# Performance work log

Measured on AMD Instinct MI355X. Metric: run time of the kernel, lower is better.

Reference implementation:

```python
import jax, jax.numpy as jnp
from jax import lax
import numpy as np
import math

INPUT_DIM = 64
HIDDEN_DIM = 512
SEQ_LEN = 256
BATCH = 512
PRED_LEN = 24
NUM_TARGETS = 1


def setup_inputs() -> dict:
    key = jax.random.key(0)
    ks = jax.random.split(key, 10)
    stdv = 1.0 / math.sqrt(HIDDEN_DIM)
    u = lambda k, shape: jax.random.uniform(k, shape, jnp.float32, -stdv, stdv)
    return {
        "x": jax.random.normal(ks[0], (BATCH, SEQ_LEN, INPUT_DIM), jnp.float32),
        "Wa": u(ks[1], (INPUT_DIM, INPUT_DIM)),
        "Ua": u(ks[2], (2 * HIDDEN_DIM, INPUT_DIM)),
        "ba": jnp.zeros((INPUT_DIM,), jnp.float32),
        "Va": u(ks[3], (INPUT_DIM, INPUT_DIM)),
        "W_ih": u(ks[4], (4 * HIDDEN_DIM, INPUT_DIM)),
        "W_hh": u(ks[5], (4 * HIDDEN_DIM, HIDDEN_DIM)),
        "b_ih": u(ks[6], (4 * HIDDEN_DIM,)),
        "b_hh": u(ks[7], (4 * HIDDEN_DIM,)),
        "fc_w": u(ks[8], (PRED_LEN * NUM_TARGETS, HIDDEN_DIM)),
        "fc_b": u(ks[9], (PRED_LEN * NUM_TARGETS,)),
    }


def reference(x, Wa, Ua, ba, Va, W_ih, W_hh, b_ih, b_hh, fc_w, fc_b):
    B, S, D = x.shape
    H = W_hh.shape[1]

    def step(carry, x_t):
        h, c = carry  # [B,H] each
        # attention gate over input features
        hc = jnp.concatenate([h, c], axis=1)  # [B,2H]
        a_t = jnp.tanh(x_t @ Wa + hc @ Ua + ba) @ Va  # [B,D]
        alpha_t = jax.nn.softmax(a_t, axis=1)
        x_att = alpha_t * x_t
        # torch.nn.LSTMCell: gates in order i, f, g, o
        gates = x_att @ W_ih.T + h @ W_hh.T + b_ih + b_hh  # [B,4H]
        i, f, g, o = jnp.split(gates, 4, axis=1)
        c_new = jax.nn.sigmoid(f) * c + jax.nn.sigmoid(i) * jnp.tanh(g)
        h_new = jax.nn.sigmoid(o) * jnp.tanh(c_new)
        return (h_new, c_new), None

    h0 = jnp.zeros((B, H), x.dtype)
    c0 = jnp.zeros((B, H), x.dtype)
    (h_T, _), _ = lax.scan(step, (h0, c0), jnp.swapaxes(x, 0, 1))  # scan over seq
    y = h_T @ fc_w.T + fc_b  # [B, pred_len*num_targets]
    return y.reshape(B, PRED_LEN, NUM_TARGETS)
```

## Files before the change

kernel.cpp:

```cpp
#include <hip/hip_runtime.h>
#include <math.h>

#define B 512
#define S 256
#define D 64
#define H 512
#define BH (B*H)

typedef __attribute__((ext_vector_type(8))) short short8;
typedef __attribute__((ext_vector_type(4))) float f32x4;
typedef __attribute__((ext_vector_type(4))) unsigned int uint4v;

__device__ inline unsigned short f2bf(float v) {
    unsigned int u = __float_as_uint(v);
    unsigned int r = (u + 0x7fffu + ((u >> 16) & 1u)) >> 16;
    return (unsigned short)r;
}
__device__ inline float bf2f(unsigned short b) {
    return __uint_as_float(((unsigned int)b) << 16);
}


__global__ __launch_bounds__(256) void init_zero(
    float* __restrict__ h32, float* __restrict__ c32)
{
    int i = blockIdx.x * blockDim.x + threadIdx.x;
    if (i < BH) { h32[i] = 0.f; c32[i] = 0.f; }
}

__global__ __launch_bounds__(256) void prep_weights(
    const float* __restrict__ Whh, const float* __restrict__ Wih,
    unsigned short* __restrict__ wswz)
{
    const int jt = blockIdx.x;
    const int kb = blockIdx.y;
    const int t = threadIdx.x;
    const int jj = t >> 3;
    const int kk8 = t & 7;
    const int jg = jt*32 + jj;
    const int u = jg >> 2, q = jg & 3;
    const int Wrow = q*H + u;

    const float* src = (kb < 8) ? (Whh + (size_t)Wrow*H + kb*64 + kk8*8)
                                : (Wih + (size_t)Wrow*D + kk8*8);
    float v[8];
    *(float4*)&v[0] = *(const float4*)(src);
    *(float4*)&v[4] = *(const float4*)(src + 4);

    unsigned short hi[8], lo[8];
    #pragma unroll
    for (int e = 0; e < 8; ++e) {
        hi[e] = f2bf(v[e]);
        lo[e] = f2bf(v[e] - bf2f(hi[e]));
    }
    const int ks = kk8 >> 2, cg2 = kk8 & 3;
    const size_t slab = (size_t)(jt*9 + kb) * 4096;
    *(short8*)(wswz + slab + (size_t)(0*2048 + ks*1024 + cg2*256 + jj*8)) = *(const short8*)hi;
    *(short8*)(wswz + slab + (size_t)(1*2048 + ks*1024 + cg2*256 + jj*8)) = *(const short8*)lo;
}

__global__ __launch_bounds__(256) void attn_kernel(
    const float* __restrict__ x, const float* __restrict__ Wa,
    const float* __restrict__ Ua, const float* __restrict__ ba,
    const float* __restrict__ Va,
    const float* __restrict__ h32, const float* __restrict__ c32,
    float* __restrict__ xatt, int t)
{
    const int d = threadIdx.x & 63;
    const int r = (threadIdx.x >> 6) & 1;
    const int p = threadIdx.x >> 7;
    const int b = blockIdx.x * 2 + r;

    const int rd = t & 1;
    const float* __restrict__ hrow = h32 + (size_t)rd*BH + (size_t)b*H;
    const float* __restrict__ crow = c32 + (size_t)b*H;
    const float* __restrict__ xrow = x + ((size_t)b*S + t)*D;

    __shared__ float part[2][2][64];
    __shared__ float ta[2][64];
    __shared__ float pv[2][2][64];

    float a = 0.f;
    if (p == 0) {
        a = ba[d];
        #pragma unroll 8
        for (int k = 0; k < D; ++k) a += xrow[k] * Wa[k*D + d];
        #pragma unroll 8
        for (int k = 0; k < H; ++k) a += hrow[k] * Ua[k*D + d];
    } else {
        #pragma unroll 8
        for (int k = 0; k < H; ++k) a += crow[k] * Ua[(size_t)(H + k)*D + d];
    }
    part[r][p][d] = a;
    __syncthreads();
    if (p == 0) ta[r][d] = tanhf(part[r][0][d] + part[r][1][d]);
    __syncthreads();
    float av = 0.f;
    {
        const int k0 = p * 32;
        #pragma unroll 8
        for (int k = k0; k < k0 + 32; ++k) av += ta[r][k] * Va[k*D + d];
    }
    pv[r][p][d] = av;
    __syncthreads();
    float v = pv[r][0][d] + pv[r][1][d];
    float m = v;
    #pragma unroll
    for (int o = 32; o > 0; o >>= 1) m = fmaxf(m, __shfl_xor(m, o));
    float e = expf(v - m);
    float ssum = e;
    #pragma unroll
    for (int o = 32; o > 0; o >>= 1) ssum += __shfl_xor(ssum, o);
    if (p == 0) {
        xatt[(size_t)b*D + d] = (e / ssum) * xrow[d];
    }
}

__global__ __launch_bounds__(256, 2) void gates_kernel(
    const unsigned short* __restrict__ wswz,
    const float* __restrict__ xatt,
    float* __restrict__ h32, float* __restrict__ c32,
    const float* __restrict__ bih, const float* __restrict__ bhh, int t)
{
    const int tid = threadIdx.x;
    const int lane = tid & 63;
    const int wid = tid >> 6;
    const int wr = wid >> 1, wc = wid & 1;
    const int jt = blockIdx.x;
    const int b0 = blockIdx.y * 64;
    const int l15 = lane & 15;
    const int cgi = lane >> 4;

    __shared__ __align__(16) unsigned short aHi[2][64][72];
    __shared__ __align__(16) unsigned short aLo[2][64][72];
    __shared__ float gout[64][37];

    const int rd = t & 1, wrs = rd ^ 1;
    const float* __restrict__ h32r = h32 + (size_t)rd*BH;

    const int srow = tid >> 2;
    const int q4 = tid & 3;

    auto stage = [&](const float* src, int buf) {
        float v[16];
        #pragma unroll
        for (int i = 0; i < 4; ++i)
            *(float4*)&v[i*4] = *(const float4*)(src + i*4);
        unsigned int hp[8], lp[8];
        #pragma unroll
        for (int w = 0; w < 8; ++w) {
            unsigned int ue = __float_as_uint(v[2*w]);
            unsigned int uo = __float_as_uint(v[2*w+1]);
            hp[w] = (ue >> 16) | (uo & 0xFFFF0000u);
            float le = v[2*w]   - __uint_as_float(ue & 0xFFFF0000u);
            float lq = v[2*w+1] - __uint_as_float(uo & 0xFFFF0000u);
            lp[w] = (__float_as_uint(le) >> 16) | (__float_as_uint(lq) & 0xFFFF0000u);
        }
        *(uint4v*)&aHi[buf][srow][q4*16]     = *(uint4v*)&hp[0];
        *(uint4v*)&aHi[buf][srow][q4*16 + 8] = *(uint4v*)&hp[4];
        *(uint4v*)&aLo[buf][srow][q4*16]     = *(uint4v*)&lp[0];
        *(uint4v*)&aLo[buf][srow][q4*16 + 8] = *(uint4v*)&lp[4];
    };

    stage(h32r + (size_t)(b0 + srow)*H + q4*16, 0);
    __syncthreads();

    f32x4 acc0 = {0,0,0,0}, acc1 = {0,0,0,0};
    const int lofs = cgi*256 + (wc*16 + l15)*8;

    for (int kb = 0; kb < 9; ++kb) {
        const int cur = kb & 1;
        const unsigned short* pB = wswz + (size_t)(jt*9 + kb)*4096;
        short8 bh0 = *(const short8*)(pB + 0*2048 + 0*1024 + lofs);
        short8 bh1 = *(const short8*)(pB + 0*2048 + 1*1024 + lofs);
        short8 bl0 = *(const short8*)(pB + 1*2048 + 0*1024 + lofs);
        short8 bl1 = *(const short8*)(pB + 1*2048 + 1*1024 + lofs);
        if (kb < 8) {
            const float* nsrc = (kb + 1 < 8)
                ? (h32r + (size_t)(b0 + srow)*H + (kb + 1)*64 + q4*16)
                : (xatt + (size_t)(b0 + srow)*D + q4*16);
            stage(nsrc, cur ^ 1);
        }
        const int ar = wr*32 + l15;
        short8 ah00 = *(const short8*)&aHi[cur][ar     ][cgi*8];
        short8 ah01 = *(const short8*)&aHi[cur][ar     ][32 + cgi*8];
        short8 ah10 = *(const short8*)&aHi[cur][ar + 16][cgi*8];
        short8 ah11 = *(const short8*)&aHi[cur][ar + 16][32 + cgi*8];
        short8 al00 = *(const short8*)&aLo[cur][ar     ][cgi*8];
        short8 al01 = *(const short8*)&aLo[cur][ar     ][32 + cgi*8];
        short8 al10 = *(const short8*)&aLo[cur][ar + 16][cgi*8];
        short8 al11 = *(const short8*)&aLo[cur][ar + 16][32 + cgi*8];

        acc0 = __builtin_amdgcn_mfma_f32_16x16x32_bf16(ah00, bh0, acc0, 0,0,0);
        acc1 = __builtin_amdgcn_mfma_f32_16x16x32_bf16(ah10, bh0, acc1, 0,0,0);
        acc0 = __builtin_amdgcn_mfma_f32_16x16x32_bf16(ah00, bl0, acc0, 0,0,0);
        acc1 = __builtin_amdgcn_mfma_f32_16x16x32_bf16(ah10, bl0, acc1, 0,0,0);
        acc0 = __builtin_amdgcn_mfma_f32_16x16x32_bf16(al00, bh0, acc0, 0,0,0);
        acc1 = __builtin_amdgcn_mfma_f32_16x16x32_bf16(al10, bh0, acc1, 0,0,0);
        acc0 = __builtin_amdgcn_mfma_f32_16x16x32_bf16(ah01, bh1, acc0, 0,0,0);
        acc1 = __builtin_amdgcn_mfma_f32_16x16x32_bf16(ah11, bh1, acc1, 0,0,0);
        acc0 = __builtin_amdgcn_mfma_f32_16x16x32_bf16(ah01, bl1, acc0, 0,0,0);
        acc1 = __builtin_amdgcn_mfma_f32_16x16x32_bf16(ah11, bl1, acc1, 0,0,0);
        acc0 = __builtin_amdgcn_mfma_f32_16x16x32_bf16(al01, bh1, acc0, 0,0,0);
        acc1 = __builtin_amdgcn_mfma_f32_16x16x32_bf16(al11, bh1, acc1, 0,0,0);
        __syncthreads();
    }

    {
        const int m0 = cgi * 4;
        #pragma unroll
        for (int r = 0; r < 4; ++r) {
            gout[wr*32 + m0 + r     ][wc*16 + l15] = acc0[r];
            gout[wr*32 + 16 + m0 + r][wc*16 + l15] = acc1[r];
        }
    }
    __syncthreads();
    {
        const int u8 = tid & 7;
        const int u_glob = jt*8 + u8;
        const float bs0 = bih[0*H + u_glob] + bhh[0*H + u_glob];
        const float bs1 = bih[1*H + u_glob] + bhh[1*H + u_glob];
        const float bs2 = bih[2*H + u_glob] + bhh[2*H + u_glob];
        const float bs3 = bih[3*H + u_glob] + bhh[3*H + u_glob];
        float* __restrict__ h32w = h32 + (size_t)wrs*BH;
        #pragma unroll
        for (int pp = 0; pp < 2; ++pp) {
            const int row_loc = (tid >> 3) + pp*32;
            const int b = b0 + row_loc;
            float gi = gout[row_loc][u8*4 + 0] + bs0;
            float gf = gout[row_loc][u8*4 + 1] + bs1;
            float gg = gout[row_loc][u8*4 + 2] + bs2;
            float go = gout[row_loc][u8*4 + 3] + bs3;
            const size_t idx = (size_t)b*H + u_glob;
            float c_old = c32[idx];
            float si = 1.f/(1.f + expf(-gi));
            float sf = 1.f/(1.f + expf(-gf));
            float so = 1.f/(1.f + expf(-go));
            float cn = sf*c_old + si*tanhf(gg);
            float hn = so*tanhf(cn);
            c32[idx] = cn;
            h32w[idx] = hn;
        }
    }
}

__global__ __launch_bounds__(256) void fc_kernel(
    const float* __restrict__ fcw, const float* __restrict__ fcb,
    const float* __restrict__ h32, float* __restrict__ out)
{
    const int b = blockIdx.x;
    __shared__ float hrow[H];
    const float* __restrict__ hp = h32 + (size_t)b*H;
    for (int k = threadIdx.x; k < H; k += 256) hrow[k] = hp[k];
    __syncthreads();
    int j = threadIdx.x;
    if (j < 24) {
        float a = fcb[j];
        #pragma unroll 8
        for (int k = 0; k < H; ++k) a += hrow[k] * fcw[j*H + k];
        out[b*24 + j] = a;
    }
}

extern "C" void kernel_launch(void* const* d_in, const int* in_sizes, int n_in,
                              void* d_out, int out_size, void* d_ws, size_t ws_size,
                              hipStream_t stream) {
    const float* x   = (const float*)d_in[0];
    const float* Wa  = (const float*)d_in[1];
    const float* Ua  = (const float*)d_in[2];
    const float* ba  = (const float*)d_in[3];
    const float* Va  = (const float*)d_in[4];
    const float* Wih = (const float*)d_in[5];
    const float* Whh = (const float*)d_in[6];
    const float* bih = (const float*)d_in[7];
    const float* bhh = (const float*)d_in[8];
    const float* fcw = (const float*)d_in[9];
    const float* fcb = (const float*)d_in[10];
    float* out = (float*)d_out;

    char* base = (char*)d_ws;
    float* h32  = (float*)(base);
    float* c32  = (float*)(base + (size_t)2*BH*4);
    float* xatt = (float*)(base + (size_t)3*BH*4);
    unsigned short* wswz = (unsigned short*)(base + (size_t)3*BH*4 + (size_t)B*D*4);

    hipLaunchKernelGGL(init_zero, dim3((BH + 255)/256), dim3(256), 0, stream,
                       h32, c32);
    hipLaunchKernelGGL(prep_weights, dim3(64, 9), dim3(256), 0, stream,
                       Whh, Wih, wswz);
    for (int t = 0; t < S; ++t) {
        hipLaunchKernelGGL(attn_kernel, dim3(B/2), dim3(256), 0, stream,
                           x, Wa, Ua, ba, Va, h32, c32, xatt, t);
        hipLaunchKernelGGL(gates_kernel, dim3(64, 8), dim3(256), 0, stream,
                           wswz, xatt, h32, c32, bih, bhh, t);
    }
    hipLaunchKernelGGL(fc_kernel, dim3(B), dim3(256), 0, stream, fcw, fcb, h32, out);
}
```

Measured before the change: 7.906 ms.

## Replace split-bf16 MFMA gates GEMM with FP32 FMA tiling and restructure attention

The gates GEMM no longer uses split-bf16 MFMA with pre-swizzled weights. It now uses a plain FP32 register-tiled SIMT GEMM that reads the fp32 W_hh/W_ih directly into double-buffered LDS, which removes the prep_weights pass. The attention kernel is reorganised to process 4 batch rows per block, with the concatenated x/h/c rows staged in LDS and the K dimension split across waves. Dropping the matrix cores costs a lot of arithmetic throughput on a 512x2048x576 GEMM per step, though it gives exact fp32 accumulation.

Result: slower. 27.61 ms (+249.3%).

```diff
diff --git a/kernel.cpp b/kernel.cpp
--- a/kernel.cpp
+++ b/kernel.cpp
@@ -7,56 +7,12 @@
 #define H 512
 #define BH (B*H)
 
-typedef __attribute__((ext_vector_type(8))) short short8;
-typedef __attribute__((ext_vector_type(4))) float f32x4;
-typedef __attribute__((ext_vector_type(4))) unsigned int uint4v;
-
-__device__ inline unsigned short f2bf(float v) {
-    unsigned int u = __float_as_uint(v);
-    unsigned int r = (u + 0x7fffu + ((u >> 16) & 1u)) >> 16;
-    return (unsigned short)r;
-}
-__device__ inline float bf2f(unsigned short b) {
-    return __uint_as_float(((unsigned int)b) << 16);
-}
-
 
 __global__ __launch_bounds__(256) void init_zero(
     float* __restrict__ h32, float* __restrict__ c32)
 {
     int i = blockIdx.x * blockDim.x + threadIdx.x;
     if (i < BH) { h32[i] = 0.f; c32[i] = 0.f; }
-}
-
-__global__ __launch_bounds__(256) void prep_weights(
-    const float* __restrict__ Whh, const float* __restrict__ Wih,
-    unsigned short* __restrict__ wswz)
-{
-    const int jt = blockIdx.x;
-    const int kb = blockIdx.y;
-    const int t = threadIdx.x;
-    const int jj = t >> 3;
-    const int kk8 = t & 7;
-    const int jg = jt*32 + jj;
-    const int u = jg >> 2, q = jg & 3;
-    const int Wrow = q*H + u;
-
-    const float* src = (kb < 8) ? (Whh + (size_t)Wrow*H + kb*64 + kk8*8)
-                                : (Wih + (size_t)Wrow*D + kk8*8);
-    float v[8];
-    *(float4*)&v[0] = *(const float4*)(src);
-    *(float4*)&v[4] = *(const float4*)(src + 4);
-
-    unsigned short hi[8], lo[8];
-    #pragma unroll
-    for (int e = 0; e < 8; ++e) {
-        hi[e] = f2bf(v[e]);
-        lo[e] = f2bf(v[e] - bf2f(hi[e]));
-    }
-    const int ks = kk8 >> 2, cg2 = kk8 & 3;
-    const size_t slab = (size_t)(jt*9 + kb) * 4096;
-    *(short8*)(wswz + slab + (size_t)(0*2048 + ks*1024 + cg2*256 + jj*8)) = *(const short8*)hi;
-    *(short8*)(wswz + slab + (size_t)(1*2048 + ks*1024 + cg2*256 + jj*8)) = *(const short8*)lo;
 }
 
 __global__ __launch_bounds__(256) void attn_kernel(
@@ -66,181 +22,208 @@
     const float* __restrict__ h32, const float* __restrict__ c32,
     float* __restrict__ xatt, int t)
 {
-    const int d = threadIdx.x & 63;
-    const int r = (threadIdx.x >> 6) & 1;
-    const int p = threadIdx.x >> 7;
-    const int b = blockIdx.x * 2 + r;
-
-    const int rd = t & 1;
-    const float* __restrict__ hrow = h32 + (size_t)rd*BH + (size_t)b*H;
-    const float* __restrict__ crow = c32 + (size_t)b*H;
-    const float* __restrict__ xrow = x + ((size_t)b*S + t)*D;
-
-    __shared__ float part[2][2][64];
-    __shared__ float ta[2][64];
-    __shared__ float pv[2][2][64];
-
-    float a = 0.f;
-    if (p == 0) {
-        a = ba[d];
-        #pragma unroll 8
-        for (int k = 0; k < D; ++k) a += xrow[k] * Wa[k*D + d];
-        #pragma unroll 8
-        for (int k = 0; k < H; ++k) a += hrow[k] * Ua[k*D + d];
-    } else {
-        #pragma unroll 8
-        for (int k = 0; k < H; ++k) a += crow[k] * Ua[(size_t)(H + k)*D + d];
-    }
-    part[r][p][d] = a;
-    __syncthreads();
-    if (p == 0) ta[r][d] = tanhf(part[r][0][d] + part[r][1][d]);
-    __syncthreads();
-    float av = 0.f;
-    {
-        const int k0 = p * 32;
-        #pragma unroll 8
-        for (int k = k0; k < k0 + 32; ++k) av += ta[r][k] * Va[k*D + d];
-    }
-    pv[r][p][d] = av;
-    __syncthreads();
-    float v = pv[r][0][d] + pv[r][1][d];
-    float m = v;
-    #pragma unroll
-    for (int o = 32; o > 0; o >>= 1) m = fmaxf(m, __shfl_xor(m, o));
-    float e = expf(v - m);
-    float ssum = e;
-    #pragma unroll
-    for (int o = 32; o > 0; o >>= 1) ssum += __shfl_xor(ssum, o);
-    if (p == 0) {
-        xatt[(size_t)b*D + d] = (e / ssum) * xrow[d];
-    }
-}
-
-__global__ __launch_bounds__(256, 2) void gates_kernel(
-    const unsigned short* __restrict__ wswz,
-    const float* __restrict__ xatt,
-    float* __restrict__ h32, float* __restrict__ c32,
-    const float* __restrict__ bih, const float* __restrict__ bhh, int t)
-{
     const int tid = threadIdx.x;
     const int lane = tid & 63;
-    const int wid = tid >> 6;
-    const int wr = wid >> 1, wc = wid & 1;
-    const int jt = blockIdx.x;
-    const int b0 = blockIdx.y * 64;
-    const int l15 = lane & 15;
-    const int cgi = lane >> 4;
-
-    __shared__ __align__(16) unsigned short aHi[2][64][72];
-    __shared__ __align__(16) unsigned short aLo[2][64][72];
-    __shared__ float gout[64][37];
+    const int w = tid >> 6;
+    const int b0 = blockIdx.x * 4;
+    const int rd = t & 1;
+
+    __shared__ float hc[4][1092];
+    __shared__ float part[4][4][64];
+    __shared__ float ta[4][64];
+
+    {
+        const float4* xs = (const float4*)(x + ((size_t)(b0 + w)*S + t)*D);
+        const float4* hs = (const float4*)(h32 + (size_t)rd*BH + (size_t)(b0 + w)*H);
+        const float4* cs = (const float4*)(c32 + (size_t)(b0 + w)*H);
+        for (int c = lane; c < 272; c += 64) {
+            float4 v;
+            if (c < 16)       v = xs[c];
+            else if (c < 144) v = hs[c - 16];
+            else              v = cs[c - 144];
+            *(float4*)&hc[w][c*4] = v;
+        }
+    }
+    __syncthreads();
+
+    {
+        const int d = lane;
+        const int k0 = w * 272;
+        float a0 = 0.f, a1 = 0.f, a2 = 0.f, a3 = 0.f;
+        #pragma unroll 4
+        for (int kk = 0; kk < 272; kk += 4) {
+            const int k = k0 + kk;
+            float uv0 = (k     < 64) ? Wa[(k    )*D + d] : Ua[(size_t)(k      - 64)*D + d];
+            float uv1 = (k + 1 < 64) ? Wa[(k + 1)*D + d] : Ua[(size_t)(k + 1 - 64)*D + d];
+            float uv2 = (k + 2 < 64) ? Wa[(k + 2)*D + d] : Ua[(size_t)(k + 2 - 64)*D + d];
+            float uv3 = (k + 3 < 64) ? Wa[(k + 3)*D + d] : Ua[(size_t)(k + 3 - 64)*D + d];
+            float4 h0 = *(const float4*)&hc[0][k];
+            float4 h1 = *(const float4*)&hc[1][k];
+            float4 h2 = *(const float4*)&hc[2][k];
+            float4 h3 = *(const float4*)&hc[3][k];
+            a0 = fmaf(h0.x, uv0, a0); a0 = fmaf(h0.y, uv1, a0);
+            a0 = fmaf(h0.z, uv2, a0); a0 = fmaf(h0.w, uv3, a0);
+            a1 = fmaf(h1.x, uv0, a1); a1 = fmaf(h1.y, uv1, a1);
+            a1 = fmaf(h1.z, uv2, a1); a1 = fmaf(h1.w, uv3, a1);
+            a2 = fmaf(h2.x, uv0, a2); a2 = fmaf(h2.y, uv1, a2);
+            a2 = fmaf(h2.z, uv2, a2); a2 = fmaf(h2.w, uv3, a2);
+            a3 = fmaf(h3.x, uv0, a3); a3 = fmaf(h3.y, uv1, a3);
+            a3 = fmaf(h3.z, uv2, a3); a3 = fmaf(h3.w, uv3, a3);
+        }
+        part[w][0][d] = a0;
+        part[w][1][d] = a1;
+        part[w][2][d] = a2;
+        part[w][3][d] = a3;
+    }
+    __syncthreads();
+    {
+        float pre = ba[lane] + part[0][w][lane] + part[1][w][lane]
+                  + part[2][w][lane] + part[3][w][lane];
+        ta[w][lane] = tanhf(pre);
+    }
+    __syncthreads();
+    {
+        const int d = lane;
+        float av = 0.f;
+        #pragma unroll
+        for (int k = 0; k < 64; k += 4) {
+            float4 tv = *(const float4*)&ta[w][k];
+            av = fmaf(tv.x, Va[(k    )*D + d], av);
+            av = fmaf(tv.y, Va[(k + 1)*D + d], av);
+            av = fmaf(tv.z, Va[(k + 2)*D + d], av);
+            av = fmaf(tv.w, Va[(k + 3)*D + d], av);
+        }
+        float m = av;
+        #pragma unroll
+        for (int o = 32; o > 0; o >>= 1) m = fmaxf(m, __shfl_xor(m, o));
+        float e = expf(av - m);
+        float ssum = e;
+        #pragma unroll
+        for (int o = 32; o > 0; o >>= 1) ssum += __shfl_xor(ssum, o);
+        xatt[(size_t)(b0 + w)*D + d] = (e / ssum) * hc[w][d];
+    }
+}
+
+__global__ __launch_bounds__(256) void gates_kernel(
+    const float* __restrict__ Wih, const float* __restrict__ Whh,
+    const float* __restrict__ bih, const float* __restrict__ bhh,
+    const float* __restrict__ xatt, float* __restrict__ h32,
+    float* __restrict__ c32, int t)
+{
+    const int tid = threadIdx.x;
+    const int tm = tid & 7;
+    const int tn = tid >> 3;
+    const int u0 = blockIdx.x * 32;
+    const int r0 = blockIdx.y * 32;
+    const int u  = u0 + tn;
+
+    __shared__ float h_lds[2][32][68];
+    __shared__ float w_lds[2][4][32][68];
 
     const int rd = t & 1, wrs = rd ^ 1;
-    const float* __restrict__ h32r = h32 + (size_t)rd*BH;
-
-    const int srow = tid >> 2;
-    const int q4 = tid & 3;
-
-    auto stage = [&](const float* src, int buf) {
-        float v[16];
-        #pragma unroll
-        for (int i = 0; i < 4; ++i)
-            *(float4*)&v[i*4] = *(const float4*)(src + i*4);
-        unsigned int hp[8], lp[8];
-        #pragma unroll
-        for (int w = 0; w < 8; ++w) {
-            unsigned int ue = __float_as_uint(v[2*w]);
-            unsigned int uo = __float_as_uint(v[2*w+1]);
-            hp[w] = (ue >> 16) | (uo & 0xFFFF0000u);
-            float le = v[2*w]   - __uint_as_float(ue & 0xFFFF0000u);
-            float lq = v[2*w+1] - __uint_as_float(uo & 0xFFFF0000u);
-            lp[w] = (__float_as_uint(le) >> 16) | (__float_as_uint(lq) & 0xFFFF0000u);
-        }
-        *(uint4v*)&aHi[buf][srow][q4*16]     = *(uint4v*)&hp[0];
-        *(uint4v*)&aHi[buf][srow][q4*16 + 8] = *(uint4v*)&hp[4];
-        *(uint4v*)&aLo[buf][srow][q4*16]     = *(uint4v*)&lp[0];
-        *(uint4v*)&aLo[buf][srow][q4*16 + 8] = *(uint4v*)&lp[4];
-    };
-
-    stage(h32r + (size_t)(b0 + srow)*H + q4*16, 0);
-    __syncthreads();
-
-    f32x4 acc0 = {0,0,0,0}, acc1 = {0,0,0,0};
-    const int lofs = cgi*256 + (wc*16 + l15)*8;
+    const float* __restrict__ hbuf_r = h32 + (size_t)rd*BH;
+    float* __restrict__ hbuf_w = h32 + (size_t)wrs*BH;
+
+    float acc[4][4];
+    #pragma unroll
+    for (int i = 0; i < 4; ++i)
+        #pragma unroll
+        for (int q = 0; q < 4; ++q) acc[i][q] = 0.f;
+
+    float4 wreg[8];
+    float4 hreg[2];
+
+    auto issueW = [&](int kb) {
+        #pragma unroll
+        for (int it = 0; it < 8; ++it) {
+            int j = tid + it*256;
+            int f4c = j & 15, row = j >> 4;
+            int uu = row & 31, q = row >> 5;
+            const float* src = (kb < 8)
+                ? Whh + (size_t)(q*H + u0 + uu)*H + kb*64 + f4c*4
+                : Wih + (size_t)(q*H + u0 + uu)*D + f4c*4;
+            wreg[it] = *(const float4*)src;
+        }
+    };
+    auto writeW = [&](int buf) {
+        #pragma unroll
+        for (int it = 0; it < 8; ++it) {
+            int j = tid + it*256;
+            int f4c = j & 15, row = j >> 4;
+            int uu = row & 31, q = row >> 5;
+            *(float4*)&w_lds[buf][q][uu][f4c*4] = wreg[it];
+        }
+    };
+    auto issueH = [&](int kb) {
+        #pragma unroll
+        for (int it = 0; it < 2; ++it) {
+            int j = tid + it*256;
+            int f4c = j & 15, rl = j >> 4;
+            const float* src = (kb < 8)
+                ? hbuf_r + (size_t)(r0 + rl)*H + kb*64 + f4c*4
+                : xatt + (size_t)(r0 + rl)*D + f4c*4;
+            hreg[it] = *(const float4*)src;
+        }
+    };
+    auto writeH = [&](int buf) {
+        #pragma unroll
+        for (int it = 0; it < 2; ++it) {
+            int j = tid + it*256;
+            int f4c = j & 15, rl = j >> 4;
+            *(float4*)&h_lds[buf][rl][f4c*4] = hreg[it];
+        }
+    };
+
+    issueW(0); issueH(0);
+    writeW(0); writeH(0);
+    __syncthreads();
 
     for (int kb = 0; kb < 9; ++kb) {
-        const int cur = kb & 1;
-        const unsigned short* pB = wswz + (size_t)(jt*9 + kb)*4096;
-        short8 bh0 = *(const short8*)(pB + 0*2048 + 0*1024 + lofs);
-        short8 bh1 = *(const short8*)(pB + 0*2048 + 1*1024 + lofs);
-        short8 bl0 = *(const short8*)(pB + 1*2048 + 0*1024 + lofs);
-        short8 bl1 = *(const short8*)(pB + 1*2048 + 1*1024 + lofs);
-        if (kb < 8) {
-            const float* nsrc = (kb + 1 < 8)
-                ? (h32r + (size_t)(b0 + srow)*H + (kb + 1)*64 + q4*16)
-                : (xatt + (size_t)(b0 + srow)*D + q4*16);
-            stage(nsrc, cur ^ 1);
-        }
-        const int ar = wr*32 + l15;
-        short8 ah00 = *(const short8*)&aHi[cur][ar     ][cgi*8];
-        short8 ah01 = *(const short8*)&aHi[cur][ar     ][32 + cgi*8];
-        short8 ah10 = *(const short8*)&aHi[cur][ar + 16][cgi*8];
-        short8 ah11 = *(const short8*)&aHi[cur][ar + 16][32 + cgi*8];
-        short8 al00 = *(const short8*)&aLo[cur][ar     ][cgi*8];
-        short8 al01 = *(const short8*)&aLo[cur][ar     ][32 + cgi*8];
-        short8 al10 = *(const short8*)&aLo[cur][ar + 16][cgi*8];
-        short8 al11 = *(const short8*)&aLo[cur][ar + 16][32 + cgi*8];
-
-        acc0 = __builtin_amdgcn_mfma_f32_16x16x32_bf16(ah00, bh0, acc0, 0,0,0);
-        acc1 = __builtin_amdgcn_mfma_f32_16x16x32_bf16(ah10, bh0, acc1, 0,0,0);
-        acc0 = __builtin_amdgcn_mfma_f32_16x16x32_bf16(ah00, bl0, acc0, 0,0,0);
-        acc1 = __builtin_amdgcn_mfma_f32_16x16x32_bf16(ah10, bl0, acc1, 0,0,0);
-        acc0 = __builtin_amdgcn_mfma_f32_16x16x32_bf16(al00, bh0, acc0, 0,0,0);
-        acc1 = __builtin_amdgcn_mfma_f32_16x16x32_bf16(al10, bh0, acc1, 0,0,0);
-        acc0 = __builtin_amdgcn_mfma_f32_16x16x32_bf16(ah01, bh1, acc0, 0,0,0);
-        acc1 = __builtin_amdgcn_mfma_f32_16x16x32_bf16(ah11, bh1, acc1, 0,0,0);
-        acc0 = __builtin_amdgcn_mfma_f32_16x16x32_bf16(ah01, bl1, acc0, 0,0,0);
-        acc1 = __builtin_amdgcn_mfma_f32_16x16x32_bf16(ah11, bl1, acc1, 0,0,0);
-        acc0 = __builtin_amdgcn_mfma_f32_16x16x32_bf16(al01, bh1, acc0, 0,0,0);
-        acc1 = __builtin_amdgcn_mfma_f32_16x16x32_bf16(al11, bh1, acc1, 0,0,0);
+        const int buf = kb & 1;
+        if (kb < 8) { issueW(kb + 1); issueH(kb + 1); }
+        #pragma unroll
+        for (int k4 = 0; k4 < 16; ++k4) {
+            float4 wv[4], hv[4];
+            #pragma unroll
+            for (int q = 0; q < 4; ++q)
+                wv[q] = *(const float4*)&w_lds[buf][q][tn][k4*4];
+            #pragma unroll
+            for (int i = 0; i < 4; ++i)
+                hv[i] = *(const float4*)&h_lds[buf][tm + 8*i][k4*4];
+            #pragma unroll
+            for (int i = 0; i < 4; ++i)
+                #pragma unroll
+                for (int q = 0; q < 4; ++q) {
+                    acc[i][q] = fmaf(hv[i].x, wv[q].x, acc[i][q]);
+                    acc[i][q] = fmaf(hv[i].y, wv[q].y, acc[i][q]);
+                    acc[i][q] = fmaf(hv[i].z, wv[q].z, acc[i][q]);
+                    acc[i][q] = fmaf(hv[i].w, wv[q].w, acc[i][q]);
+                }
+        }
+        if (kb < 8) { writeW(buf ^ 1); writeH(buf ^ 1); }
         __syncthreads();
     }
 
-    {
-        const int m0 = cgi * 4;
-        #pragma unroll
-        for (int r = 0; r < 4; ++r) {
-            gout[wr*32 + m0 + r     ][wc*16 + l15] = acc0[r];
-            gout[wr*32 + 16 + m0 + r][wc*16 + l15] = acc1[r];
-        }
-    }
-    __syncthreads();
-    {
-        const int u8 = tid & 7;
-        const int u_glob = jt*8 + u8;
-        const float bs0 = bih[0*H + u_glob] + bhh[0*H + u_glob];
-        const float bs1 = bih[1*H + u_glob] + bhh[1*H + u_glob];
-        const float bs2 = bih[2*H + u_glob] + bhh[2*H + u_glob];
-        const float bs3 = bih[3*H + u_glob] + bhh[3*H + u_glob];
-        float* __restrict__ h32w = h32 + (size_t)wrs*BH;
-        #pragma unroll
-        for (int pp = 0; pp < 2; ++pp) {
-            const int row_loc = (tid >> 3) + pp*32;
-            const int b = b0 + row_loc;
-            float gi = gout[row_loc][u8*4 + 0] + bs0;
-            float gf = gout[row_loc][u8*4 + 1] + bs1;
-            float gg = gout[row_loc][u8*4 + 2] + bs2;
-            float go = gout[row_loc][u8*4 + 3] + bs3;
-            const size_t idx = (size_t)b*H + u_glob;
-            float c_old = c32[idx];
-            float si = 1.f/(1.f + expf(-gi));
-            float sf = 1.f/(1.f + expf(-gf));
-            float so = 1.f/(1.f + expf(-go));
-            float cn = sf*c_old + si*tanhf(gg);
-            float hn = so*tanhf(cn);
-            c32[idx] = cn;
-            h32w[idx] = hn;
-        }
+    float bsum[4];
+    #pragma unroll
+    for (int q = 0; q < 4; ++q) bsum[q] = bih[q*H + u] + bhh[q*H + u];
+
+    #pragma unroll
+    for (int i = 0; i < 4; ++i) {
+        int b = r0 + tm + 8*i;
+        float gi = acc[i][0] + bsum[0];
+        float gf = acc[i][1] + bsum[1];
+        float gg = acc[i][2] + bsum[2];
+        float go = acc[i][3] + bsum[3];
+        const size_t idx = (size_t)b*H + u;
+        float c_old = c32[idx];
+        float si = 1.f / (1.f + expf(-gi));
+        float sf = 1.f / (1.f + expf(-gf));
+        float so = 1.f / (1.f + expf(-go));
+        float cn = sf * c_old + si * tanhf(gg);
+        float hn = so * tanhf(cn);
+        c32[idx] = cn;
+        hbuf_w[idx] = hn;
     }
 }
 
@@ -282,17 +265,14 @@
     float* h32  = (float*)(base);
     float* c32  = (float*)(base + (size_t)2*BH*4);
     float* xatt = (float*)(base + (size_t)3*BH*4);
-    unsigned short* wswz = (unsigned short*)(base + (size_t)3*BH*4 + (size_t)B*D*4);
 
     hipLaunchKernelGGL(init_zero, dim3((BH + 255)/256), dim3(256), 0, stream,
                        h32, c32);
-    hipLaunchKernelGGL(prep_weights, dim3(64, 9), dim3(256), 0, stream,
-                       Whh, Wih, wswz);
     for (int t = 0; t < S; ++t) {
-        hipLaunchKernelGGL(attn_kernel, dim3(B/2), dim3(256), 0, stream,
+        hipLaunchKernelGGL(attn_kernel, dim3(B/4), dim3(256), 0, stream,
                            x, Wa, Ua, ba, Va, h32, c32, xatt, t);
-        hipLaunchKernelGGL(gates_kernel, dim3(64, 8), dim3(256), 0, stream,
-                           wswz, xatt, h32, c32, bih, bhh, t);
+        hipLaunchKernelGGL(gates_kernel, dim3(16, 16), dim3(256), 0, stream,
+                           Wih, Whh, bih, bhh, xatt, h32, c32, t);
     }
     hipLaunchKernelGGL(fc_kernel, dim3(B), dim3(256), 0, stream, fcw, fcb, h32, out);
 }
```
